# Kernel tuning notes

Measured on AMD Instinct MI355X. Metric: run time of the kernel, lower is better.

## Reference

```python
import jax, jax.numpy as jnp
import numpy as np

B, T, I, H, O = 128, 1024, 1, 512, 1


def setup_inputs() -> dict:
    key = jax.random.key(0)
    k = jax.random.split(key, 6)
    s = 1.0 / np.sqrt(H).astype(np.float32)
    x = jax.random.normal(k[0], (B, T, I), dtype=jnp.float32)
    Wx = jax.random.uniform(k[1], (I, 4 * H), jnp.float32, -s, s)   # input->gates
    Wh = jax.random.uniform(k[2], (H, 4 * H), jnp.float32, -s, s)   # hidden->gates
    b = jax.random.uniform(k[3], (4 * H,), jnp.float32, -s, s)      # gate bias
    Wl = jax.random.uniform(k[4], (H, O), jnp.float32, -s, s)       # readout
    bl = jax.random.uniform(k[5], (O,), jnp.float32, -s, s)
    return {"x": x, "Wx": Wx, "Wh": Wh, "b": b, "Wl": Wl, "bl": bl, "future": 0}


def reference(x, Wx, Wh, b, Wl, bl, future):
    # x: (B, T, I). Custom LSTM cell unrolled over time via lax.scan, with a
    # per-timestep linear readout (as in the original per-step loop).
    H_ = Wh.shape[0]
    h0 = jnp.zeros((x.shape[0], H_), dtype=x.dtype)
    c0 = jnp.zeros((x.shape[0], H_), dtype=x.dtype)

    def step(carry, xt):  # xt: (B, I)
        h, c = carry
        gates = xt @ Wx + h @ Wh + b            # (B, 4H)
        i, f, g, o = jnp.split(gates, 4, axis=-1)
        i = jax.nn.sigmoid(i)
        f = jax.nn.sigmoid(f)
        g = jnp.tanh(g)
        o = jax.nn.sigmoid(o)
        c = f * c + i * g
        h = o * jnp.tanh(c)
        y = h @ Wl + bl                          # (B, O)
        return (h, c), y

    (_, _), ys = jax.lax.scan(step, (h0, c0), jnp.swapaxes(x, 0, 1))
    # ys: (T, B, O) -> (B, T, O), matching torch.stack(outputs,1).squeeze(2)
    return jnp.swapaxes(ys, 0, 1)
```

## Files before the change

### kernel.cpp

```cpp
#include <hip/hip_runtime.h>
#include <hip/hip_fp16.h>


typedef _Float16 f16;
typedef _Float16 f16x2 __attribute__((ext_vector_type(2)));
typedef _Float16 f16x8 __attribute__((ext_vector_type(8)));
typedef float f32x4 __attribute__((ext_vector_type(4)));

#define BATCH 128
#define TT 1024
#define HID 512

#define WPACK_OFF   0
#define WPACK_BYTES (32*4*16*64*16)
#define HBUF_OFF    (WPACK_OFF + WPACK_BYTES)
#define HBUF_ELEMS  (BATCH*HID)
#define WL16_OFF    (HBUF_OFF + 4*HBUF_ELEMS*2)

__global__ __launch_bounds__(256) void init_kernel(const float* Wl, f16* wl16,
                                                   unsigned* hbuf) {
    int idx = blockIdx.x * 256 + threadIdx.x;
    hbuf[idx] = ((idx >> 15) == 0) ? 0u : 0x00010001u;
    if (idx < HID) wl16[idx] = (f16)Wl[idx];
}

__global__ __launch_bounds__(256) void pack_kernel(const float* __restrict__ Wh,
                                                   f16* __restrict__ wpack) {
    int tid  = blockIdx.x * 256 + threadIdx.x;
    int lane = tid & 63;
    int s    = (tid >> 6) & 15;
    int wv   = (tid >> 10) & 3;
    int cg   = tid >> 12;
    int l_lo = lane & 15, l_hi = lane >> 4;
    int jt = ((wv * 4) + s) & 15;
    int jj = l_lo >> 2, q = l_lo & 3;
    int c = q * 512 + cg * 16 + wv * 4 + jj;
    int kbase = jt * 32 + l_hi * 8;
    f16x8 v;
#pragma unroll
    for (int e = 0; e < 8; ++e) v[e] = (f16)Wh[(kbase + e) * 2048 + c];
    ((f16x8*)wpack)[tid] = v;
}

__device__ __forceinline__ float dot8(f16x8 a, f16x8 b, float acc) {
#if __has_builtin(__builtin_amdgcn_fdot2)
    acc = __builtin_amdgcn_fdot2(__builtin_shufflevector(a, a, 0, 1),
                                 __builtin_shufflevector(b, b, 0, 1), acc, false);
    acc = __builtin_amdgcn_fdot2(__builtin_shufflevector(a, a, 2, 3),
                                 __builtin_shufflevector(b, b, 2, 3), acc, false);
    acc = __builtin_amdgcn_fdot2(__builtin_shufflevector(a, a, 4, 5),
                                 __builtin_shufflevector(b, b, 4, 5), acc, false);
    acc = __builtin_amdgcn_fdot2(__builtin_shufflevector(a, a, 6, 7),
                                 __builtin_shufflevector(b, b, 6, 7), acc, false);
#else
#pragma unroll
    for (int e = 0; e < 8; ++e) acc += (float)a[e] * (float)b[e];
#endif
    return acc;
}

__global__ __launch_bounds__(256, 1) void lstm_kernel(
    const float* __restrict__ x, const float* __restrict__ Wx,
    const float* __restrict__ bvec, const float* __restrict__ blp,
    const f16* __restrict__ wpack, f16* __restrict__ hbuf,
    const f16* __restrict__ wl16, float* __restrict__ out)
{
    const int tid = threadIdx.x;
    const int cg = blockIdx.x >> 3;
    const int bg = blockIdx.x & 7;
    const int w = tid >> 6, lane = tid & 63;
    const int l_lo = lane & 15, l_hi = lane >> 4;

    __shared__ f16 hsh[2][8192];
    __shared__ f16 wlsh[512];

    if (tid < 64)
        *(f16x8*)(wlsh + tid * 8) = *(const f16x8*)(wl16 + tid * 8);

    f16x8 bf[16];
    {
        const f16x8* wp = (const f16x8*)wpack + (size_t)((cg * 4 + w) * 16) * 64 + lane;
#pragma unroll
        for (int s = 0; s < 16; ++s) bf[s] = wp[s * 64];
    }

    const int row  = l_hi * 4 + (l_lo & 3);
    const int uglob = cg * 16 + w * 4 + (l_lo >> 2);
    const int bglob = bg * 16 + row;
    const float bias_i = bvec[0*512+uglob], bias_f = bvec[1*512+uglob];
    const float bias_g = bvec[2*512+uglob], bias_o = bvec[3*512+uglob];
    const float wx_i = Wx[0*512+uglob], wx_f = Wx[1*512+uglob];
    const float wx_g = Wx[2*512+uglob], wx_o = Wx[3*512+uglob];
    const float blv = blp[0];

    const int rd_base = bg * 8192 + ((w * 16 + l_hi) * 16 + l_lo) * 8;
    const int st_idx = bg * 8192 + ((uglob >> 3) * 16 + row) * 8 + (uglob & 7);

    const int p4 = l_lo & 3;
    const int sx = (l_lo & 7) << 4;
    const int lbase = l_lo * 1024;
    const int base_ws = w * 256 + l_hi * 16;
    const int xrow = bglob * TT;

    float cst = 0.f;

    for (int t = 0; t <= TT; ++t) {
        const f16* hp = hbuf + (size_t)(t & 3) * HBUF_ELEMS + rd_base;
        const unsigned expect = (unsigned)((t >> 2) & 1);
        float xv = x[xrow + (t < TT ? t : 0)];

        f16x8 s0, s1, s2, s3;
        for (;;) {
            asm volatile(
                "global_load_dwordx4 %0, %4, off sc0 sc1\n\t"
                "global_load_dwordx4 %1, %5, off sc0 sc1\n\t"
                "global_load_dwordx4 %2, %6, off sc0 sc1\n\t"
                "global_load_dwordx4 %3, %7, off sc0 sc1\n\t"
                "s_waitcnt vmcnt(0)"
                : "=&v"(s0), "=&v"(s1), "=&v"(s2), "=&v"(s3)
                : "v"(hp), "v"(hp + 512), "v"(hp + 1024), "v"(hp + 1536)
                : "memory");
            union { f16x8 v; unsigned u[4]; } a0, a1, a2, a3;
            a0.v = s0; a1.v = s1; a2.v = s2; a3.v = s3;
            unsigned bad =
                ((a0.u[0] ^ expect) | (a0.u[1] ^ expect) |
                 (a0.u[2] ^ expect) | (a0.u[3] ^ expect) |
                 (a1.u[0] ^ expect) | (a1.u[1] ^ expect) |
                 (a1.u[2] ^ expect) | (a1.u[3] ^ expect) |
                 (a2.u[0] ^ expect) | (a2.u[1] ^ expect) |
                 (a2.u[2] ^ expect) | (a2.u[3] ^ expect) |
                 (a3.u[0] ^ expect) | (a3.u[1] ^ expect) |
                 (a3.u[2] ^ expect) | (a3.u[3] ^ expect)) & 1u;
            if (__all(bad == 0u)) break;
        }
        __builtin_amdgcn_sched_barrier(0);

        char* hb = (char*)hsh[t & 1];
        const int wb = lbase + base_ws;
        *(f16x8*)(hb + ((wb +   0) ^ sx)) = s0;
        *(f16x8*)(hb + ((wb +  64) ^ sx)) = s1;
        *(f16x8*)(hb + ((wb + 128) ^ sx)) = s2;
        *(f16x8*)(hb + ((wb + 192) ^ sx)) = s3;

        f32x4 c0 = {0,0,0,0};
        if (t < TT) {
            c0 = __builtin_amdgcn_mfma_f32_16x16x32_f16(s0, bf[0], c0, 0,0,0);
            c0 = __builtin_amdgcn_mfma_f32_16x16x32_f16(s1, bf[1], c0, 0,0,0);
            c0 = __builtin_amdgcn_mfma_f32_16x16x32_f16(s2, bf[2], c0, 0,0,0);
            c0 = __builtin_amdgcn_mfma_f32_16x16x32_f16(s3, bf[3], c0, 0,0,0);
        }
        __syncthreads();

        if (t < TT) {
            f32x4 c1 = {0,0,0,0}, c2 = {0,0,0,0}, c3 = {0,0,0,0};
#pragma unroll
            for (int i = 0; i < 4; ++i) {
                f16x8 a1 = *(const f16x8*)(hb + ((lbase + ((base_ws + (4+i)*64) & 1023)) ^ sx));
                f16x8 a2 = *(const f16x8*)(hb + ((lbase + ((base_ws + (8+i)*64) & 1023)) ^ sx));
                f16x8 a3 = *(const f16x8*)(hb + ((lbase + ((base_ws + (12+i)*64) & 1023)) ^ sx));
                c1 = __builtin_amdgcn_mfma_f32_16x16x32_f16(a1, bf[ 4+i], c1, 0,0,0);
                c2 = __builtin_amdgcn_mfma_f32_16x16x32_f16(a2, bf[ 8+i], c2, 0,0,0);
                c3 = __builtin_amdgcn_mfma_f32_16x16x32_f16(a3, bf[12+i], c3, 0,0,0);
            }
            f32x4 m = (c0 + c1) + (c2 + c3);

            float t0, e0, e1, e2, e3, f0, f1, f2, f3;
            t0 = __shfl_xor(m[1], 1); e0 = (p4 & 1) ? t0 : m[0];
            t0 = __shfl_xor(m[0], 1); e1 = (p4 & 1) ? m[1] : t0;
            t0 = __shfl_xor(m[3], 1); e2 = (p4 & 1) ? t0 : m[2];
            t0 = __shfl_xor(m[2], 1); e3 = (p4 & 1) ? m[3] : t0;
            t0 = __shfl_xor(e2, 2); f0 = (p4 & 2) ? t0 : e0;
            t0 = __shfl_xor(e3, 2); f1 = (p4 & 2) ? t0 : e1;
            t0 = __shfl_xor(e0, 2); f2 = (p4 & 2) ? e2 : t0;
            t0 = __shfl_xor(e1, 2); f3 = (p4 & 2) ? e3 : t0;

            float gi = f0 + xv * wx_i + bias_i;
            float gf = f1 + xv * wx_f + bias_f;
            float gg = f2 + xv * wx_g + bias_g;
            float go = f3 + xv * wx_o + bias_o;
            float iv = 1.f / (1.f + __expf(-gi));
            float fv = 1.f / (1.f + __expf(-gf));
            float gv = 2.f / (1.f + __expf(-2.f * gg)) - 1.f;
            float ov = 1.f / (1.f + __expf(-go));
            cst = fv * cst + iv * gv;
            float hv = ov * (2.f / (1.f + __expf(-2.f * cst)) - 1.f);

            unsigned hval;
            { union { f16 f; unsigned short s; } cv; cv.f = (f16)hv; hval = cv.s; }
            unsigned hodd = __shfl_xor(hval, 4);
            const unsigned wtag = (unsigned)(((t + 1) >> 2) & 1);
            if ((l_lo & 4) == 0) {
                unsigned dw = ((hval | (hodd << 16)) & ~1u) | wtag;
                f16* dst = hbuf + (size_t)((t + 1) & 3) * HBUF_ELEMS + st_idx;
                asm volatile("global_store_dword %0, %1, off sc0 sc1"
                             :: "v"(dst), "v"(dw) : "memory");
            }
        }

        if (t >= 1 && cg == ((t >> 2) & 31) && w == (t & 3)) {
            float r0 = 0.f, r1 = 0.f, r2 = 0.f, r3 = 0.f;
            r0 = dot8(s0, *(const f16x8*)(wlsh + (((base_ws + 0*64) & 1023) >> 1)), r0);
            r1 = dot8(s1, *(const f16x8*)(wlsh + (((base_ws + 1*64) & 1023) >> 1)), r1);
            r2 = dot8(s2, *(const f16x8*)(wlsh + (((base_ws + 2*64) & 1023) >> 1)), r2);
            r3 = dot8(s3, *(const f16x8*)(wlsh + (((base_ws + 3*64) & 1023) >> 1)), r3);
#pragma unroll
            for (int i = 0; i < 4; ++i) {
                f16x8 a1 = *(const f16x8*)(hb + ((lbase + ((base_ws + (4+i)*64) & 1023)) ^ sx));
                f16x8 a2 = *(const f16x8*)(hb + ((lbase + ((base_ws + (8+i)*64) & 1023)) ^ sx));
                f16x8 a3 = *(const f16x8*)(hb + ((lbase + ((base_ws + (12+i)*64) & 1023)) ^ sx));
                r0 = dot8(a1, *(const f16x8*)(wlsh + (((base_ws + (4+i)*64) & 1023) >> 1)), r0);
                r1 = dot8(a2, *(const f16x8*)(wlsh + (((base_ws + (8+i)*64) & 1023) >> 1)), r1);
                r2 = dot8(a3, *(const f16x8*)(wlsh + (((base_ws + (12+i)*64) & 1023) >> 1)), r2);
            }
            float ry = (r0 + r1) + (r2 + r3);
            ry += __shfl_xor(ry, 16);
            ry += __shfl_xor(ry, 32);
            if (lane < 16)
                out[(bg * 16 + l_lo) * TT + (t - 1)] = blv + ry;
        }
    }
}

extern "C" void kernel_launch(void* const* d_in, const int* in_sizes, int n_in,
                              void* d_out, int out_size, void* d_ws, size_t ws_size,
                              hipStream_t stream) {
    const float* x  = (const float*)d_in[0];
    const float* Wx = (const float*)d_in[1];
    const float* Wh = (const float*)d_in[2];
    const float* bv = (const float*)d_in[3];
    const float* Wl = (const float*)d_in[4];
    const float* bl = (const float*)d_in[5];
    float* out = (float*)d_out;
    char* ws = (char*)d_ws;

    f16* wpack = (f16*)(ws + WPACK_OFF);
    f16* hbuf  = (f16*)(ws + HBUF_OFF);
    f16* wl16  = (f16*)(ws + WL16_OFF);

    init_kernel<<<512, 256, 0, stream>>>(Wl, wl16, (unsigned*)hbuf);
    pack_kernel<<<512, 256, 0, stream>>>(Wh, wpack);
    lstm_kernel<<<256, 256, 0, stream>>>(x, Wx, bv, bl, wpack, hbuf, wl16, out);
}
```

Baseline: 2.209 ms.

## Replace per-step workgroup barrier with tag-polled LDS exchange across waves

Removes the __syncthreads between the wave's own slice write and the reads of other waves' slices. Each wave now spins on volatile LDS loads, checking the parity tag bit embedded in the h values, and the shared staging buffer grows from two to four slots so tags stay unambiguous. The readout reuses the already loaded fragments instead of reloading from LDS. This trades the barrier for polling loops and extra LDS traffic, and relies on LDS write ordering between waves being visible in that order.

```diff
diff --git a/kernel.cpp b/kernel.cpp
--- a/kernel.cpp
+++ b/kernel.cpp
@@ -3,9 +3,9 @@
 
 
 typedef _Float16 f16;
-typedef _Float16 f16x2 __attribute__((ext_vector_type(2)));
 typedef _Float16 f16x8 __attribute__((ext_vector_type(8)));
 typedef float f32x4 __attribute__((ext_vector_type(4)));
+typedef unsigned u32x4 __attribute__((ext_vector_type(4)));
 
 #define BATCH 128
 #define TT 1024
@@ -59,6 +59,35 @@
     return acc;
 }
 
+#define FOREIGN_Q(qi, A0, A1, A2, A3, ACC)                                     \
+    do {                                                                       \
+        const int q0 = lbase + ((base_ws + ((qi)*4 + 0) * 64) & 1023);         \
+        const int q1 = lbase + ((base_ws + ((qi)*4 + 1) * 64) & 1023);         \
+        const int q2 = lbase + ((base_ws + ((qi)*4 + 2) * 64) & 1023);         \
+        const int q3 = lbase + ((base_ws + ((qi)*4 + 3) * 64) & 1023);         \
+        u32x4 v0, v1, v2, v3;                                                  \
+        for (;;) {                                                             \
+            v0 = *(volatile const u32x4*)(hb + (q0 ^ sx));                     \
+            v1 = *(volatile const u32x4*)(hb + (q1 ^ sx));                     \
+            v2 = *(volatile const u32x4*)(hb + (q2 ^ sx));                     \
+            v3 = *(volatile const u32x4*)(hb + (q3 ^ sx));                     \
+            unsigned bad =                                                     \
+                ((v0[0]^expect)|(v0[1]^expect)|(v0[2]^expect)|(v0[3]^expect) | \
+                 (v1[0]^expect)|(v1[1]^expect)|(v1[2]^expect)|(v1[3]^expect) | \
+                 (v2[0]^expect)|(v2[1]^expect)|(v2[2]^expect)|(v2[3]^expect) | \
+                 (v3[0]^expect)|(v3[1]^expect)|(v3[2]^expect)|(v3[3]^expect))  \
+                & 1u;                                                          \
+            if (__all(bad == 0u)) break;                                       \
+        }                                                                      \
+        union { u32x4 u; f16x8 f; } c0_, c1_, c2_, c3_;                        \
+        c0_.u = v0; c1_.u = v1; c2_.u = v2; c3_.u = v3;                        \
+        A0 = c0_.f; A1 = c1_.f; A2 = c2_.f; A3 = c3_.f;                        \
+        ACC = __builtin_amdgcn_mfma_f32_16x16x32_f16(A0, bf[(qi)*4+0], ACC, 0,0,0); \
+        ACC = __builtin_amdgcn_mfma_f32_16x16x32_f16(A1, bf[(qi)*4+1], ACC, 0,0,0); \
+        ACC = __builtin_amdgcn_mfma_f32_16x16x32_f16(A2, bf[(qi)*4+2], ACC, 0,0,0); \
+        ACC = __builtin_amdgcn_mfma_f32_16x16x32_f16(A3, bf[(qi)*4+3], ACC, 0,0,0); \
+    } while (0)
+
 __global__ __launch_bounds__(256, 1) void lstm_kernel(
     const float* __restrict__ x, const float* __restrict__ Wx,
     const float* __restrict__ bvec, const float* __restrict__ blp,
@@ -71,11 +100,17 @@
     const int w = tid >> 6, lane = tid & 63;
     const int l_lo = lane & 15, l_hi = lane >> 4;
 
-    __shared__ f16 hsh[2][8192];
+    __shared__ f16 hsh[4][8192];
     __shared__ f16 wlsh[512];
 
     if (tid < 64)
         *(f16x8*)(wlsh + tid * 8) = *(const f16x8*)(wl16 + tid * 8);
+    {
+        unsigned* p = (unsigned*)hsh;
+#pragma unroll
+        for (int i = 0; i < 64; ++i) p[tid + i * 256] = 0x00010001u;
+    }
+    __syncthreads();
 
     f16x8 bf[16];
     {
@@ -109,7 +144,7 @@
         const unsigned expect = (unsigned)((t >> 2) & 1);
         float xv = x[xrow + (t < TT ? t : 0)];
 
-        f16x8 s0, s1, s2, s3;
+        f16x8 a0, a1, a2, a3;
         for (;;) {
             asm volatile(
                 "global_load_dwordx4 %0, %4, off sc0 sc1\n\t"
@@ -117,51 +152,39 @@
                 "global_load_dwordx4 %2, %6, off sc0 sc1\n\t"
                 "global_load_dwordx4 %3, %7, off sc0 sc1\n\t"
                 "s_waitcnt vmcnt(0)"
-                : "=&v"(s0), "=&v"(s1), "=&v"(s2), "=&v"(s3)
+                : "=&v"(a0), "=&v"(a1), "=&v"(a2), "=&v"(a3)
                 : "v"(hp), "v"(hp + 512), "v"(hp + 1024), "v"(hp + 1536)
                 : "memory");
-            union { f16x8 v; unsigned u[4]; } a0, a1, a2, a3;
-            a0.v = s0; a1.v = s1; a2.v = s2; a3.v = s3;
+            union { f16x8 v; unsigned u[4]; } b0, b1, b2, b3;
+            b0.v = a0; b1.v = a1; b2.v = a2; b3.v = a3;
             unsigned bad =
-                ((a0.u[0] ^ expect) | (a0.u[1] ^ expect) |
-                 (a0.u[2] ^ expect) | (a0.u[3] ^ expect) |
-                 (a1.u[0] ^ expect) | (a1.u[1] ^ expect) |
-                 (a1.u[2] ^ expect) | (a1.u[3] ^ expect) |
-                 (a2.u[0] ^ expect) | (a2.u[1] ^ expect) |
-                 (a2.u[2] ^ expect) | (a2.u[3] ^ expect) |
-                 (a3.u[0] ^ expect) | (a3.u[1] ^ expect) |
-                 (a3.u[2] ^ expect) | (a3.u[3] ^ expect)) & 1u;
+                ((b0.u[0]^expect)|(b0.u[1]^expect)|(b0.u[2]^expect)|(b0.u[3]^expect) |
+                 (b1.u[0]^expect)|(b1.u[1]^expect)|(b1.u[2]^expect)|(b1.u[3]^expect) |
+                 (b2.u[0]^expect)|(b2.u[1]^expect)|(b2.u[2]^expect)|(b2.u[3]^expect) |
+                 (b3.u[0]^expect)|(b3.u[1]^expect)|(b3.u[2]^expect)|(b3.u[3]^expect)) & 1u;
             if (__all(bad == 0u)) break;
         }
         __builtin_amdgcn_sched_barrier(0);
 
-        char* hb = (char*)hsh[t & 1];
+        char* hb = (char*)hsh[t & 3];
         const int wb = lbase + base_ws;
-        *(f16x8*)(hb + ((wb +   0) ^ sx)) = s0;
-        *(f16x8*)(hb + ((wb +  64) ^ sx)) = s1;
-        *(f16x8*)(hb + ((wb + 128) ^ sx)) = s2;
-        *(f16x8*)(hb + ((wb + 192) ^ sx)) = s3;
-
-        f32x4 c0 = {0,0,0,0};
+        *(volatile f16x8*)(hb + ((wb +   0) ^ sx)) = a0;
+        *(volatile f16x8*)(hb + ((wb +  64) ^ sx)) = a1;
+        *(volatile f16x8*)(hb + ((wb + 128) ^ sx)) = a2;
+        *(volatile f16x8*)(hb + ((wb + 192) ^ sx)) = a3;
+
+        f32x4 c0 = {0,0,0,0}, c1 = {0,0,0,0}, c2 = {0,0,0,0}, c3 = {0,0,0,0};
+        c0 = __builtin_amdgcn_mfma_f32_16x16x32_f16(a0, bf[0], c0, 0,0,0);
+        c0 = __builtin_amdgcn_mfma_f32_16x16x32_f16(a1, bf[1], c0, 0,0,0);
+        c0 = __builtin_amdgcn_mfma_f32_16x16x32_f16(a2, bf[2], c0, 0,0,0);
+        c0 = __builtin_amdgcn_mfma_f32_16x16x32_f16(a3, bf[3], c0, 0,0,0);
+
+        f16x8 a4, a5, a6, a7, a8, a9, a10, a11, a12, a13, a14, a15;
+        FOREIGN_Q(1, a4,  a5,  a6,  a7,  c1);
+        FOREIGN_Q(2, a8,  a9,  a10, a11, c2);
+        FOREIGN_Q(3, a12, a13, a14, a15, c3);
+
         if (t < TT) {
-            c0 = __builtin_amdgcn_mfma_f32_16x16x32_f16(s0, bf[0], c0, 0,0,0);
-            c0 = __builtin_amdgcn_mfma_f32_16x16x32_f16(s1, bf[1], c0, 0,0,0);
-            c0 = __builtin_amdgcn_mfma_f32_16x16x32_f16(s2, bf[2], c0, 0,0,0);
-            c0 = __builtin_amdgcn_mfma_f32_16x16x32_f16(s3, bf[3], c0, 0,0,0);
-        }
-        __syncthreads();
-
-        if (t < TT) {
-            f32x4 c1 = {0,0,0,0}, c2 = {0,0,0,0}, c3 = {0,0,0,0};
-#pragma unroll
-            for (int i = 0; i < 4; ++i) {
-                f16x8 a1 = *(const f16x8*)(hb + ((lbase + ((base_ws + (4+i)*64) & 1023)) ^ sx));
-                f16x8 a2 = *(const f16x8*)(hb + ((lbase + ((base_ws + (8+i)*64) & 1023)) ^ sx));
-                f16x8 a3 = *(const f16x8*)(hb + ((lbase + ((base_ws + (12+i)*64) & 1023)) ^ sx));
-                c1 = __builtin_amdgcn_mfma_f32_16x16x32_f16(a1, bf[ 4+i], c1, 0,0,0);
-                c2 = __builtin_amdgcn_mfma_f32_16x16x32_f16(a2, bf[ 8+i], c2, 0,0,0);
-                c3 = __builtin_amdgcn_mfma_f32_16x16x32_f16(a3, bf[12+i], c3, 0,0,0);
-            }
             f32x4 m = (c0 + c1) + (c2 + c3);
 
             float t0, e0, e1, e2, e3, f0, f1, f2, f3;
@@ -199,19 +222,16 @@
 
         if (t >= 1 && cg == ((t >> 2) & 31) && w == (t & 3)) {
             float r0 = 0.f, r1 = 0.f, r2 = 0.f, r3 = 0.f;
-            r0 = dot8(s0, *(const f16x8*)(wlsh + (((base_ws + 0*64) & 1023) >> 1)), r0);
-            r1 = dot8(s1, *(const f16x8*)(wlsh + (((base_ws + 1*64) & 1023) >> 1)), r1);
-            r2 = dot8(s2, *(const f16x8*)(wlsh + (((base_ws + 2*64) & 1023) >> 1)), r2);
-            r3 = dot8(s3, *(const f16x8*)(wlsh + (((base_ws + 3*64) & 1023) >> 1)), r3);
-#pragma unroll
-            for (int i = 0; i < 4; ++i) {
-                f16x8 a1 = *(const f16x8*)(hb + ((lbase + ((base_ws + (4+i)*64) & 1023)) ^ sx));
-                f16x8 a2 = *(const f16x8*)(hb + ((lbase + ((base_ws + (8+i)*64) & 1023)) ^ sx));
-                f16x8 a3 = *(const f16x8*)(hb + ((lbase + ((base_ws + (12+i)*64) & 1023)) ^ sx));
-                r0 = dot8(a1, *(const f16x8*)(wlsh + (((base_ws + (4+i)*64) & 1023) >> 1)), r0);
-                r1 = dot8(a2, *(const f16x8*)(wlsh + (((base_ws + (8+i)*64) & 1023) >> 1)), r1);
-                r2 = dot8(a3, *(const f16x8*)(wlsh + (((base_ws + (12+i)*64) & 1023) >> 1)), r2);
-            }
+#define WL(s) (*(const f16x8*)(wlsh + (((base_ws + (s)*64) & 1023) >> 1)))
+            r0 = dot8(a0,  WL(0),  r0); r1 = dot8(a1,  WL(1),  r1);
+            r2 = dot8(a2,  WL(2),  r2); r3 = dot8(a3,  WL(3),  r3);
+            r0 = dot8(a4,  WL(4),  r0); r1 = dot8(a5,  WL(5),  r1);
+            r2 = dot8(a6,  WL(6),  r2); r3 = dot8(a7,  WL(7),  r3);
+            r0 = dot8(a8,  WL(8),  r0); r1 = dot8(a9,  WL(9),  r1);
+            r2 = dot8(a10, WL(10), r2); r3 = dot8(a11, WL(11), r3);
+            r0 = dot8(a12, WL(12), r0); r1 = dot8(a13, WL(13), r1);
+            r2 = dot8(a14, WL(14), r2); r3 = dot8(a15, WL(15), r3);
+#undef WL
             float ry = (r0 + r1) + (r2 + r3);
             ry += __shfl_xor(ry, 16);
             ry += __shfl_xor(ry, 32);
```

Result: slower. 3.026 ms (+36.9%).

## Poll a shadow hidden-state buffer with device-scope loads, falling back to system scope

Applied to the files above, without the earlier changes.

Adds a second (shadow) copy of the hidden-state ring buffer. Every step's h values are written to both copies. The cross-block spin-wait first polls the shadow copy using sc0-only loads, which have narrower coherence scope and may be cheaper. After too many failed polls it permanently switches to the original sc0 sc1 loads. The aim is to cut the latency of the inter-block handoff on each timestep. The cost is doubled store traffic, and there is a risk that the narrower-scope loads read stale data across XCDs, which would trigger the slow fallback.

```diff
diff --git a/kernel.cpp b/kernel.cpp
--- a/kernel.cpp
+++ b/kernel.cpp
@@ -3,7 +3,6 @@
 
 
 typedef _Float16 f16;
-typedef _Float16 f16x2 __attribute__((ext_vector_type(2)));
 typedef _Float16 f16x8 __attribute__((ext_vector_type(8)));
 typedef float f32x4 __attribute__((ext_vector_type(4)));
 
@@ -15,12 +14,16 @@
 #define WPACK_BYTES (32*4*16*64*16)
 #define HBUF_OFF    (WPACK_OFF + WPACK_BYTES)
 #define HBUF_ELEMS  (BATCH*HID)
-#define WL16_OFF    (HBUF_OFF + 4*HBUF_ELEMS*2)
+#define SHBUF_OFF   (HBUF_OFF + 4*HBUF_ELEMS*2)
+#define WL16_OFF    (SHBUF_OFF + 4*HBUF_ELEMS*2)
+#define FALLBACK_THRESH 128
 
 __global__ __launch_bounds__(256) void init_kernel(const float* Wl, f16* wl16,
-                                                   unsigned* hbuf) {
+                                                   unsigned* hbuf, unsigned* hsh) {
     int idx = blockIdx.x * 256 + threadIdx.x;
-    hbuf[idx] = ((idx >> 15) == 0) ? 0u : 0x00010001u;
+    unsigned v = ((idx >> 15) == 0) ? 0u : 0x00010001u;
+    hbuf[idx] = v;
+    hsh[idx]  = v;
     if (idx < HID) wl16[idx] = (f16)Wl[idx];
 }
 
@@ -63,7 +66,8 @@
     const float* __restrict__ x, const float* __restrict__ Wx,
     const float* __restrict__ bvec, const float* __restrict__ blp,
     const f16* __restrict__ wpack, f16* __restrict__ hbuf,
-    const f16* __restrict__ wl16, float* __restrict__ out)
+    f16* __restrict__ hshadow, const f16* __restrict__ wl16,
+    float* __restrict__ out)
 {
     const int tid = threadIdx.x;
     const int cg = blockIdx.x >> 3;
@@ -103,35 +107,47 @@
     const int xrow = bglob * TT;
 
     float cst = 0.f;
+    int fails = 0;
+    bool useLLC = false;
 
     for (int t = 0; t <= TT; ++t) {
-        const f16* hp = hbuf + (size_t)(t & 3) * HBUF_ELEMS + rd_base;
+        const f16* hp  = hbuf    + (size_t)(t & 3) * HBUF_ELEMS + rd_base;
+        const f16* hpS = hshadow + (size_t)(t & 3) * HBUF_ELEMS + rd_base;
         const unsigned expect = (unsigned)((t >> 2) & 1);
         float xv = x[xrow + (t < TT ? t : 0)];
 
         f16x8 s0, s1, s2, s3;
         for (;;) {
-            asm volatile(
-                "global_load_dwordx4 %0, %4, off sc0 sc1\n\t"
-                "global_load_dwordx4 %1, %5, off sc0 sc1\n\t"
-                "global_load_dwordx4 %2, %6, off sc0 sc1\n\t"
-                "global_load_dwordx4 %3, %7, off sc0 sc1\n\t"
-                "s_waitcnt vmcnt(0)"
-                : "=&v"(s0), "=&v"(s1), "=&v"(s2), "=&v"(s3)
-                : "v"(hp), "v"(hp + 512), "v"(hp + 1024), "v"(hp + 1536)
-                : "memory");
-            union { f16x8 v; unsigned u[4]; } a0, a1, a2, a3;
-            a0.v = s0; a1.v = s1; a2.v = s2; a3.v = s3;
+            if (!useLLC) {
+                asm volatile(
+                    "global_load_dwordx4 %0, %4, off sc0\n\t"
+                    "global_load_dwordx4 %1, %5, off sc0\n\t"
+                    "global_load_dwordx4 %2, %6, off sc0\n\t"
+                    "global_load_dwordx4 %3, %7, off sc0\n\t"
+                    "s_waitcnt vmcnt(0)"
+                    : "=&v"(s0), "=&v"(s1), "=&v"(s2), "=&v"(s3)
+                    : "v"(hpS), "v"(hpS + 512), "v"(hpS + 1024), "v"(hpS + 1536)
+                    : "memory");
+            } else {
+                asm volatile(
+                    "global_load_dwordx4 %0, %4, off sc0 sc1\n\t"
+                    "global_load_dwordx4 %1, %5, off sc0 sc1\n\t"
+                    "global_load_dwordx4 %2, %6, off sc0 sc1\n\t"
+                    "global_load_dwordx4 %3, %7, off sc0 sc1\n\t"
+                    "s_waitcnt vmcnt(0)"
+                    : "=&v"(s0), "=&v"(s1), "=&v"(s2), "=&v"(s3)
+                    : "v"(hp), "v"(hp + 512), "v"(hp + 1024), "v"(hp + 1536)
+                    : "memory");
+            }
+            union { f16x8 v; unsigned u[4]; } b0, b1, b2, b3;
+            b0.v = s0; b1.v = s1; b2.v = s2; b3.v = s3;
             unsigned bad =
-                ((a0.u[0] ^ expect) | (a0.u[1] ^ expect) |
-                 (a0.u[2] ^ expect) | (a0.u[3] ^ expect) |
-                 (a1.u[0] ^ expect) | (a1.u[1] ^ expect) |
-                 (a1.u[2] ^ expect) | (a1.u[3] ^ expect) |
-                 (a2.u[0] ^ expect) | (a2.u[1] ^ expect) |
-                 (a2.u[2] ^ expect) | (a2.u[3] ^ expect) |
-                 (a3.u[0] ^ expect) | (a3.u[1] ^ expect) |
-                 (a3.u[2] ^ expect) | (a3.u[3] ^ expect)) & 1u;
-            if (__all(bad == 0u)) break;
+                ((b0.u[0]^expect)|(b0.u[1]^expect)|(b0.u[2]^expect)|(b0.u[3]^expect) |
+                 (b1.u[0]^expect)|(b1.u[1]^expect)|(b1.u[2]^expect)|(b1.u[3]^expect) |
+                 (b2.u[0]^expect)|(b2.u[1]^expect)|(b2.u[2]^expect)|(b2.u[3]^expect) |
+                 (b3.u[0]^expect)|(b3.u[1]^expect)|(b3.u[2]^expect)|(b3.u[3]^expect)) & 1u;
+            if (__all(bad == 0u)) { fails = 0; break; }
+            if (!useLLC && ++fails > FALLBACK_THRESH) useLLC = true;
         }
         __builtin_amdgcn_sched_barrier(0);
 
@@ -191,7 +207,10 @@
             const unsigned wtag = (unsigned)(((t + 1) >> 2) & 1);
             if ((l_lo & 4) == 0) {
                 unsigned dw = ((hval | (hodd << 16)) & ~1u) | wtag;
-                f16* dst = hbuf + (size_t)((t + 1) & 3) * HBUF_ELEMS + st_idx;
+                f16* dst  = hbuf    + (size_t)((t + 1) & 3) * HBUF_ELEMS + st_idx;
+                f16* dstS = hshadow + (size_t)((t + 1) & 3) * HBUF_ELEMS + st_idx;
+                asm volatile("global_store_dword %0, %1, off sc0"
+                             :: "v"(dstS), "v"(dw) : "memory");
                 asm volatile("global_store_dword %0, %1, off sc0 sc1"
                              :: "v"(dst), "v"(dw) : "memory");
             }
@@ -199,19 +218,21 @@
 
         if (t >= 1 && cg == ((t >> 2) & 31) && w == (t & 3)) {
             float r0 = 0.f, r1 = 0.f, r2 = 0.f, r3 = 0.f;
-            r0 = dot8(s0, *(const f16x8*)(wlsh + (((base_ws + 0*64) & 1023) >> 1)), r0);
-            r1 = dot8(s1, *(const f16x8*)(wlsh + (((base_ws + 1*64) & 1023) >> 1)), r1);
-            r2 = dot8(s2, *(const f16x8*)(wlsh + (((base_ws + 2*64) & 1023) >> 1)), r2);
-            r3 = dot8(s3, *(const f16x8*)(wlsh + (((base_ws + 3*64) & 1023) >> 1)), r3);
+#define WL(s) (*(const f16x8*)(wlsh + (((base_ws + (s)*64) & 1023) >> 1)))
+            r0 = dot8(s0, WL(0), r0);
+            r1 = dot8(s1, WL(1), r1);
+            r2 = dot8(s2, WL(2), r2);
+            r3 = dot8(s3, WL(3), r3);
 #pragma unroll
             for (int i = 0; i < 4; ++i) {
                 f16x8 a1 = *(const f16x8*)(hb + ((lbase + ((base_ws + (4+i)*64) & 1023)) ^ sx));
                 f16x8 a2 = *(const f16x8*)(hb + ((lbase + ((base_ws + (8+i)*64) & 1023)) ^ sx));
                 f16x8 a3 = *(const f16x8*)(hb + ((lbase + ((base_ws + (12+i)*64) & 1023)) ^ sx));
-                r0 = dot8(a1, *(const f16x8*)(wlsh + (((base_ws + (4+i)*64) & 1023) >> 1)), r0);
-                r1 = dot8(a2, *(const f16x8*)(wlsh + (((base_ws + (8+i)*64) & 1023) >> 1)), r1);
-                r2 = dot8(a3, *(const f16x8*)(wlsh + (((base_ws + (12+i)*64) & 1023) >> 1)), r2);
-            }
+                r0 = dot8(a1, WL(4+i),  r0);
+                r1 = dot8(a2, WL(8+i),  r1);
+                r2 = dot8(a3, WL(12+i), r2);
+            }
+#undef WL
             float ry = (r0 + r1) + (r2 + r3);
             ry += __shfl_xor(ry, 16);
             ry += __shfl_xor(ry, 32);
@@ -233,11 +254,14 @@
     float* out = (float*)d_out;
     char* ws = (char*)d_ws;
 
-    f16* wpack = (f16*)(ws + WPACK_OFF);
-    f16* hbuf  = (f16*)(ws + HBUF_OFF);
-    f16* wl16  = (f16*)(ws + WL16_OFF);
-
-    init_kernel<<<512, 256, 0, stream>>>(Wl, wl16, (unsigned*)hbuf);
+    f16* wpack   = (f16*)(ws + WPACK_OFF);
+    f16* hbuf    = (f16*)(ws + HBUF_OFF);
+    f16* hshadow = (f16*)(ws + SHBUF_OFF);
+    f16* wl16    = (f16*)(ws + WL16_OFF);
+
+    init_kernel<<<512, 256, 0, stream>>>(Wl, wl16, (unsigned*)hbuf,
+                                         (unsigned*)hshadow);
     pack_kernel<<<512, 256, 0, stream>>>(Wh, wpack);
-    lstm_kernel<<<256, 256, 0, stream>>>(x, Wx, bv, bl, wpack, hbuf, wl16, out);
-}
+    lstm_kernel<<<256, 256, 0, stream>>>(x, Wx, bv, bl, wpack, hbuf, hshadow,
+                                         wl16, out);
+}
```

Result: slower. 2.354 ms (+6.5%).

## Split readout into separate kernel via h history buffer, use DPP and per-element tags

Applied to the files above, without the earlier changes.

When the workspace is large enough, the recurrent kernel stops computing the per-step readout inline. It writes each h_t to a full history buffer, and a separate kernel then computes all readouts in parallel. This moves the readout dot product off the serial critical path, at the cost of writing and re-reading about 128 MB of fp16 history. It also replaces cross-lane shuffles with quad-permute DPP, and switches the h exchange to 16-bit stores, each carrying its own tag bit, so the lane-pair shuffle before the store is no longer needed.

```diff
diff --git a/kernel.cpp b/kernel.cpp
--- a/kernel.cpp
+++ b/kernel.cpp
@@ -3,7 +3,6 @@
 
 
 typedef _Float16 f16;
-typedef _Float16 f16x2 __attribute__((ext_vector_type(2)));
 typedef _Float16 f16x8 __attribute__((ext_vector_type(8)));
 typedef float f32x4 __attribute__((ext_vector_type(4)));
 
@@ -13,9 +12,12 @@
 
 #define WPACK_OFF   0
 #define WPACK_BYTES (32*4*16*64*16)
-#define HBUF_OFF    (WPACK_OFF + WPACK_BYTES)
+#define HBUF_OFF    WPACK_BYTES
 #define HBUF_ELEMS  (BATCH*HID)
 #define WL16_OFF    (HBUF_OFF + 4*HBUF_ELEMS*2)
+#define HHIST_OFF   (WL16_OFF + 4096)
+#define HHIST_BYTES ((size_t)TT * BATCH * HID * 2)
+#define WS_NEEDED   ((size_t)HHIST_OFF + HHIST_BYTES)
 
 __global__ __launch_bounds__(256) void init_kernel(const float* Wl, f16* wl16,
                                                    unsigned* hbuf) {
@@ -59,11 +61,20 @@
     return acc;
 }
 
+template<int CTRL>
+__device__ __forceinline__ float dpp_qp(float v) {
+    int r = __builtin_amdgcn_update_dpp(0, __builtin_bit_cast(int, v),
+                                        CTRL, 0xF, 0xF, true);
+    return __builtin_bit_cast(float, r);
+}
+
+template<int MODE>
 __global__ __launch_bounds__(256, 1) void lstm_kernel(
     const float* __restrict__ x, const float* __restrict__ Wx,
     const float* __restrict__ bvec, const float* __restrict__ blp,
     const f16* __restrict__ wpack, f16* __restrict__ hbuf,
-    const f16* __restrict__ wl16, float* __restrict__ out)
+    const f16* __restrict__ wl16, f16* __restrict__ hhist,
+    float* __restrict__ out)
 {
     const int tid = threadIdx.x;
     const int cg = blockIdx.x >> 3;
@@ -95,6 +106,7 @@
 
     const int rd_base = bg * 8192 + ((w * 16 + l_hi) * 16 + l_lo) * 8;
     const int st_idx = bg * 8192 + ((uglob >> 3) * 16 + row) * 8 + (uglob & 7);
+    const int hist_off = (bg * 16 + row) * 512 + uglob;
 
     const int p4 = l_lo & 3;
     const int sx = (l_lo & 7) << 4;
@@ -103,10 +115,11 @@
     const int xrow = bglob * TT;
 
     float cst = 0.f;
-
-    for (int t = 0; t <= TT; ++t) {
+    const int TLAST = (MODE == 0) ? (TT - 1) : TT;
+
+    for (int t = 0; t <= TLAST; ++t) {
         const f16* hp = hbuf + (size_t)(t & 3) * HBUF_ELEMS + rd_base;
-        const unsigned expect = (unsigned)((t >> 2) & 1);
+        const unsigned ep = (unsigned)((t >> 2) & 1) * 0x00010001u;
         float xv = x[xrow + (t < TT ? t : 0)];
 
         f16x8 s0, s1, s2, s3;
@@ -120,17 +133,13 @@
                 : "=&v"(s0), "=&v"(s1), "=&v"(s2), "=&v"(s3)
                 : "v"(hp), "v"(hp + 512), "v"(hp + 1024), "v"(hp + 1536)
                 : "memory");
-            union { f16x8 v; unsigned u[4]; } a0, a1, a2, a3;
-            a0.v = s0; a1.v = s1; a2.v = s2; a3.v = s3;
+            union { f16x8 v; unsigned u[4]; } b0, b1, b2, b3;
+            b0.v = s0; b1.v = s1; b2.v = s2; b3.v = s3;
             unsigned bad =
-                ((a0.u[0] ^ expect) | (a0.u[1] ^ expect) |
-                 (a0.u[2] ^ expect) | (a0.u[3] ^ expect) |
-                 (a1.u[0] ^ expect) | (a1.u[1] ^ expect) |
-                 (a1.u[2] ^ expect) | (a1.u[3] ^ expect) |
-                 (a2.u[0] ^ expect) | (a2.u[1] ^ expect) |
-                 (a2.u[2] ^ expect) | (a2.u[3] ^ expect) |
-                 (a3.u[0] ^ expect) | (a3.u[1] ^ expect) |
-                 (a3.u[2] ^ expect) | (a3.u[3] ^ expect)) & 1u;
+                (((b0.u[0]^ep)|(b0.u[1]^ep)|(b0.u[2]^ep)|(b0.u[3]^ep)) |
+                 ((b1.u[0]^ep)|(b1.u[1]^ep)|(b1.u[2]^ep)|(b1.u[3]^ep)) |
+                 ((b2.u[0]^ep)|(b2.u[1]^ep)|(b2.u[2]^ep)|(b2.u[3]^ep)) |
+                 ((b3.u[0]^ep)|(b3.u[1]^ep)|(b3.u[2]^ep)|(b3.u[3]^ep))) & 0x00010001u;
             if (__all(bad == 0u)) break;
         }
         __builtin_amdgcn_sched_barrier(0);
@@ -165,14 +174,14 @@
             f32x4 m = (c0 + c1) + (c2 + c3);
 
             float t0, e0, e1, e2, e3, f0, f1, f2, f3;
-            t0 = __shfl_xor(m[1], 1); e0 = (p4 & 1) ? t0 : m[0];
-            t0 = __shfl_xor(m[0], 1); e1 = (p4 & 1) ? m[1] : t0;
-            t0 = __shfl_xor(m[3], 1); e2 = (p4 & 1) ? t0 : m[2];
-            t0 = __shfl_xor(m[2], 1); e3 = (p4 & 1) ? m[3] : t0;
-            t0 = __shfl_xor(e2, 2); f0 = (p4 & 2) ? t0 : e0;
-            t0 = __shfl_xor(e3, 2); f1 = (p4 & 2) ? t0 : e1;
-            t0 = __shfl_xor(e0, 2); f2 = (p4 & 2) ? e2 : t0;
-            t0 = __shfl_xor(e1, 2); f3 = (p4 & 2) ? e3 : t0;
+            t0 = dpp_qp<0xB1>(m[1]); e0 = (p4 & 1) ? t0 : m[0];
+            t0 = dpp_qp<0xB1>(m[0]); e1 = (p4 & 1) ? m[1] : t0;
+            t0 = dpp_qp<0xB1>(m[3]); e2 = (p4 & 1) ? t0 : m[2];
+            t0 = dpp_qp<0xB1>(m[2]); e3 = (p4 & 1) ? m[3] : t0;
+            t0 = dpp_qp<0x4E>(e2); f0 = (p4 & 2) ? t0 : e0;
+            t0 = dpp_qp<0x4E>(e3); f1 = (p4 & 2) ? t0 : e1;
+            t0 = dpp_qp<0x4E>(e0); f2 = (p4 & 2) ? e2 : t0;
+            t0 = dpp_qp<0x4E>(e1); f3 = (p4 & 2) ? e3 : t0;
 
             float gi = f0 + xv * wx_i + bias_i;
             float gf = f1 + xv * wx_f + bias_f;
@@ -187,37 +196,69 @@
 
             unsigned hval;
             { union { f16 f; unsigned short s; } cv; cv.f = (f16)hv; hval = cv.s; }
-            unsigned hodd = __shfl_xor(hval, 4);
-            const unsigned wtag = (unsigned)(((t + 1) >> 2) & 1);
-            if ((l_lo & 4) == 0) {
-                unsigned dw = ((hval | (hodd << 16)) & ~1u) | wtag;
+
+            if ((MODE == 0) ? (t < TT - 1) : true) {
+                const unsigned wtag = (unsigned)(((t + 1) >> 2) & 1);
+                unsigned tagged = (hval & 0xFFFEu) | wtag;
                 f16* dst = hbuf + (size_t)((t + 1) & 3) * HBUF_ELEMS + st_idx;
-                asm volatile("global_store_dword %0, %1, off sc0 sc1"
-                             :: "v"(dst), "v"(dw) : "memory");
-            }
-        }
-
-        if (t >= 1 && cg == ((t >> 2) & 31) && w == (t & 3)) {
+                asm volatile("global_store_short %0, %1, off sc0 sc1"
+                             :: "v"(dst), "v"(tagged) : "memory");
+            }
+
+            if (MODE == 0) {
+                f16* hd = hhist + (size_t)t * (BATCH * HID) + hist_off;
+                asm volatile("global_store_short %0, %1, off"
+                             :: "v"(hd), "v"(hval) : "memory");
+            }
+        }
+
+        if (MODE == 1 && t >= 1 && cg == ((t >> 2) & 31) && w == (t & 3)) {
             float r0 = 0.f, r1 = 0.f, r2 = 0.f, r3 = 0.f;
-            r0 = dot8(s0, *(const f16x8*)(wlsh + (((base_ws + 0*64) & 1023) >> 1)), r0);
-            r1 = dot8(s1, *(const f16x8*)(wlsh + (((base_ws + 1*64) & 1023) >> 1)), r1);
-            r2 = dot8(s2, *(const f16x8*)(wlsh + (((base_ws + 2*64) & 1023) >> 1)), r2);
-            r3 = dot8(s3, *(const f16x8*)(wlsh + (((base_ws + 3*64) & 1023) >> 1)), r3);
+#define WL(s) (*(const f16x8*)(wlsh + (((base_ws + (s)*64) & 1023) >> 1)))
+            r0 = dot8(s0, WL(0), r0);
+            r1 = dot8(s1, WL(1), r1);
+            r2 = dot8(s2, WL(2), r2);
+            r3 = dot8(s3, WL(3), r3);
 #pragma unroll
             for (int i = 0; i < 4; ++i) {
                 f16x8 a1 = *(const f16x8*)(hb + ((lbase + ((base_ws + (4+i)*64) & 1023)) ^ sx));
                 f16x8 a2 = *(const f16x8*)(hb + ((lbase + ((base_ws + (8+i)*64) & 1023)) ^ sx));
                 f16x8 a3 = *(const f16x8*)(hb + ((lbase + ((base_ws + (12+i)*64) & 1023)) ^ sx));
-                r0 = dot8(a1, *(const f16x8*)(wlsh + (((base_ws + (4+i)*64) & 1023) >> 1)), r0);
-                r1 = dot8(a2, *(const f16x8*)(wlsh + (((base_ws + (8+i)*64) & 1023) >> 1)), r1);
-                r2 = dot8(a3, *(const f16x8*)(wlsh + (((base_ws + (12+i)*64) & 1023) >> 1)), r2);
-            }
+                r0 = dot8(a1, WL(4+i),  r0);
+                r1 = dot8(a2, WL(8+i),  r1);
+                r2 = dot8(a3, WL(12+i), r2);
+            }
+#undef WL
             float ry = (r0 + r1) + (r2 + r3);
             ry += __shfl_xor(ry, 16);
             ry += __shfl_xor(ry, 32);
             if (lane < 16)
                 out[(bg * 16 + l_lo) * TT + (t - 1)] = blv + ry;
         }
+    }
+}
+
+__global__ __launch_bounds__(256) void readout_kernel(
+    const f16* __restrict__ hhist, const float* __restrict__ Wl,
+    const float* __restrict__ blp, float* __restrict__ out)
+{
+    int gw = (blockIdx.x * 256 + threadIdx.x) >> 6;
+    int lane = threadIdx.x & 63;
+    int b = gw >> 7;
+    int t0 = (gw & 127) * 8;
+    const float4* wp = (const float4*)(Wl + lane * 8);
+    float4 wa = wp[0], wb = wp[1];
+    float blv = blp[0];
+    const f16* hp = hhist + (size_t)t0 * (BATCH * HID) + b * HID + lane * 8;
+#pragma unroll
+    for (int j = 0; j < 8; ++j) {
+        f16x8 h8 = *(const f16x8*)(hp + (size_t)j * (BATCH * HID));
+        float p = (float)h8[0]*wa.x + (float)h8[1]*wa.y + (float)h8[2]*wa.z +
+                  (float)h8[3]*wa.w + (float)h8[4]*wb.x + (float)h8[5]*wb.y +
+                  (float)h8[6]*wb.z + (float)h8[7]*wb.w;
+        p += __shfl_xor(p, 1);  p += __shfl_xor(p, 2);  p += __shfl_xor(p, 4);
+        p += __shfl_xor(p, 8);  p += __shfl_xor(p, 16); p += __shfl_xor(p, 32);
+        if (lane == 0) out[b * TT + t0 + j] = p + blv;
     }
 }
 
@@ -236,8 +277,16 @@
     f16* wpack = (f16*)(ws + WPACK_OFF);
     f16* hbuf  = (f16*)(ws + HBUF_OFF);
     f16* wl16  = (f16*)(ws + WL16_OFF);
+    f16* hhist = (f16*)(ws + HHIST_OFF);
 
     init_kernel<<<512, 256, 0, stream>>>(Wl, wl16, (unsigned*)hbuf);
     pack_kernel<<<512, 256, 0, stream>>>(Wh, wpack);
-    lstm_kernel<<<256, 256, 0, stream>>>(x, Wx, bv, bl, wpack, hbuf, wl16, out);
-}
+    if (ws_size >= WS_NEEDED) {
+        lstm_kernel<0><<<256, 256, 0, stream>>>(x, Wx, bv, bl, wpack, hbuf,
+                                                wl16, hhist, out);
+        readout_kernel<<<4096, 256, 0, stream>>>(hhist, Wl, bl, out);
+    } else {
+        lstm_kernel<1><<<256, 256, 0, stream>>>(x, Wx, bv, bl, wpack, hbuf,
+                                                wl16, hhist, out);
+    }
+}
```

New measurement: 1.915 ms. 1.15x faster.
